# Kernel tuning notes

Hardware: AMD Instinct MI355X
Metric: run time of the kernel (lower is better)

Reference implementation:

```python
import math
import jax, jax.numpy as jnp
import numpy as np

N_HEADS = 16
D_EMBED = 1024
D_HEAD = D_EMBED // N_HEADS


def setup_inputs() -> dict:
    key = jax.random.key(0)
    k1, k2, k3, k4, k5 = jax.random.split(key, 5)
    B, S, D = 4, 2048, D_EMBED
    scale = 1.0 / math.sqrt(D)
    return {
        "x": jax.random.normal(k1, (B, S, D), dtype=jnp.float32),
        "in_proj_w": jax.random.normal(k2, (3 * D, D), dtype=jnp.float32) * scale,
        "in_proj_b": jax.random.normal(k3, (3 * D,), dtype=jnp.float32) * 0.02,
        "out_proj_w": jax.random.normal(k4, (D, D), dtype=jnp.float32) * scale,
        "out_proj_b": jax.random.normal(k5, (D,), dtype=jnp.float32) * 0.02,
        "causal_mask": 0,
    }


def reference(x, in_proj_w, in_proj_b, out_proj_w, out_proj_b, causal_mask):
    B, S, D = x.shape
    # in_proj: torch Linear -> x @ W^T + b, then chunk into q,k,v
    qkv = x @ in_proj_w.T + in_proj_b              # [B,S,3D]
    q, k, v = jnp.split(qkv, 3, axis=-1)
    # [B,S,D] -> [B,H,S,d]
    def heads(t):
        return t.reshape(B, S, N_HEADS, D_HEAD).transpose(0, 2, 1, 3)
    q, k, v = heads(q), heads(k), heads(v)
    weight = jnp.einsum("bhsd,bhtd->bhst", q, k)   # [B,H,S,S] materialized scores
    if causal_mask:
        mask = jnp.triu(jnp.ones((S, S), dtype=bool), k=1)
        weight = jnp.where(mask, -jnp.inf, weight)
    weight = jax.nn.softmax(weight / math.sqrt(D_HEAD), axis=-1)
    out = jnp.einsum("bhst,bhtd->bhsd", weight, v)  # [B,H,S,d]
    out = out.transpose(0, 2, 1, 3).reshape(B, S, D)
    return out @ out_proj_w.T + out_proj_b
```

## Files before the change

### kernel.cpp

```cpp
#include <hip/hip_runtime.h>

typedef unsigned short u16;
typedef _Float16 h8 __attribute__((ext_vector_type(8)));
typedef __fp16 fp16x2 __attribute__((ext_vector_type(2)));
typedef float f32x4 __attribute__((ext_vector_type(4)));

constexpr int B_ = 4, S_ = 2048, D_ = 1024, H_ = 16;

__device__ __forceinline__ void async16(const void* g, void* l) {
  __builtin_amdgcn_global_load_lds(
      (const __attribute__((address_space(1))) void*)g,
      (__attribute__((address_space(3))) void*)l, 16, 0, 0);
}

__device__ __forceinline__ unsigned pk2(float a, float b) {
  union { fp16x2 h; unsigned u; } c;
  c.h = __builtin_amdgcn_cvt_pkrtz(a, b);
  return c.u;
}

__device__ __forceinline__ float fexp2(float x) {
#if __has_builtin(__builtin_amdgcn_exp2f)
  return __builtin_amdgcn_exp2f(x);
#else
  return exp2f(x);
#endif
}

#define QSCALE 0.18033688011112042f

__global__ __launch_bounds__(256) void cvt3_kernel(
    const float* __restrict__ x, const float* __restrict__ wi,
    const float* __restrict__ wo, _Float16* __restrict__ xh,
    _Float16* __restrict__ wih, _Float16* __restrict__ woh)
{
  const int bid = blockIdx.x;
  const float* src;
  _Float16* dst;
  int base;
  if (bid < 8192)       { src = x;  dst = xh;  base = bid; }
  else if (bid < 11264) { src = wi; dst = wih; base = bid - 8192; }
  else                  { src = wo; dst = woh; base = bid - 11264; }
  const int i = (base * 256 + threadIdx.x) * 4;
  const float4 v = *(const float4*)(src + i);
  uint2 o;
  o.x = pk2(v.x, v.y);
  o.y = pk2(v.z, v.w);
  *(uint2*)(dst + i) = o;
}

template<bool OUT_HALF, bool SCALE_Q>
__global__ __launch_bounds__(256, 2) void gemm128p_f16(
    const _Float16* __restrict__ A, const _Float16* __restrict__ Bw,
    const float* __restrict__ bias, void* __restrict__ Cout,
    int M, int N, int K)
{
  __shared__ __align__(16) _Float16 sA[2][8192];
  __shared__ __align__(16) _Float16 sB[2][8192];

  const int tid = threadIdx.x;
  const int lane = tid & 63, w = tid >> 6;
  const int wm = w & 1, wn = w >> 1;

  const int id = blockIdx.x;
  const int cpx = gridDim.x >> 3;
  const int swz = (id & 7) * cpx + (id >> 3);
  const int nbx = N >> 7;
  const int bx = swz % nbx, by = swz / nbx;
  const int m0 = by * 128, n0 = bx * 128;

  const int r15 = lane & 15, s4 = lane >> 4;
  const int tA0 = w, tA1 = w + 4;
  const _Float16* gA0 = A + (size_t)(m0 + 16 * tA0 + r15) * K + s4 * 8;
  const _Float16* gA1 = A + (size_t)(m0 + 16 * tA1 + r15) * K + s4 * 8;
  const _Float16* gB0 = Bw + (size_t)(n0 + 16 * tA0 + r15) * K + s4 * 8;
  const _Float16* gB1 = Bw + (size_t)(n0 + 16 * tA1 + r15) * K + s4 * 8;

  auto stage = [&](int tile, int kk, int bq) {
    const int ko = tile * 64 + kk * 32;
    async16(gA0 + ko, &sA[bq][(tA0 * 2 + kk) * 512]);
    async16(gA1 + ko, &sA[bq][(tA1 * 2 + kk) * 512]);
    async16(gB0 + ko, &sB[bq][(tA0 * 2 + kk) * 512]);
    async16(gB1 + ko, &sB[bq][(tA1 * 2 + kk) * 512]);
  };

  const f32x4 zf = {0.f, 0.f, 0.f, 0.f};
  f32x4 acc[4][4];
#pragma unroll
  for (int i = 0; i < 4; ++i)
#pragma unroll
    for (int j = 0; j < 4; ++j) acc[i][j] = zf;

  const int NT = K >> 6;

  stage(0, 0, 0);
  stage(0, 1, 0);
  stage(1, 0, 1);

#define VM8 asm volatile("s_waitcnt vmcnt(8)" ::: "memory")
#define VM4 asm volatile("s_waitcnt vmcnt(4)" ::: "memory")
#define VM0 asm volatile("s_waitcnt vmcnt(0)" ::: "memory")
#define FENCE asm volatile("" ::: "memory")

  for (int T = 0; T < NT; ++T) {
    const int buf = T & 1;
    const bool lastT = (T == NT - 1);

    if (!lastT) { VM8; } else { VM4; }
    __builtin_amdgcn_s_barrier();
    FENCE;
    {
      h8 fa[4], fb[4];
#pragma unroll
      for (int i = 0; i < 4; ++i) {
        fa[i] = *(const h8*)&sA[buf][((wm * 4 + i) * 2 + 0) * 512 + lane * 8];
        fb[i] = *(const h8*)&sB[buf][((wn * 4 + i) * 2 + 0) * 512 + lane * 8];
      }
      if (T + 1 < NT) stage(T + 1, 1, (T + 1) & 1);
      __builtin_amdgcn_s_setprio(1);
#pragma unroll
      for (int i = 0; i < 4; ++i)
#pragma unroll
        for (int j = 0; j < 4; ++j)
          acc[i][j] = __builtin_amdgcn_mfma_f32_16x16x32_f16(fa[i], fb[j], acc[i][j], 0, 0, 0);
      __builtin_amdgcn_s_setprio(0);
    }

    if (!lastT) { VM8; } else { VM0; }
    __builtin_amdgcn_s_barrier();
    FENCE;
    {
      h8 fa[4], fb[4];
#pragma unroll
      for (int i = 0; i < 4; ++i) {
        fa[i] = *(const h8*)&sA[buf][((wm * 4 + i) * 2 + 1) * 512 + lane * 8];
        fb[i] = *(const h8*)&sB[buf][((wn * 4 + i) * 2 + 1) * 512 + lane * 8];
      }
      if (T + 2 < NT) stage(T + 2, 0, buf);
      __builtin_amdgcn_s_setprio(1);
#pragma unroll
      for (int i = 0; i < 4; ++i)
#pragma unroll
        for (int j = 0; j < 4; ++j)
          acc[i][j] = __builtin_amdgcn_mfma_f32_16x16x32_f16(fa[i], fb[j], acc[i][j], 0, 0, 0);
      __builtin_amdgcn_s_setprio(0);
    }
  }

#undef VM8
#undef VM4
#undef VM0
#undef FENCE

  const int g = lane >> 4, cc = lane & 15;
#pragma unroll
  for (int j = 0; j < 4; ++j) {
    const int col = n0 + (wn * 4 + j) * 16 + cc;
    const float bv = bias[col];
    float qs = 1.0f;
    if constexpr (SCALE_Q) qs = (col < 1024) ? QSCALE : 1.0f;
#pragma unroll
    for (int i = 0; i < 4; ++i) {
      const int rowb = m0 + (wm * 4 + i) * 16 + g * 4;
#pragma unroll
      for (int r = 0; r < 4; ++r) {
        float v = acc[i][j][r] + bv;
        if constexpr (SCALE_Q) v *= qs;
        if constexpr (OUT_HALF)
          ((_Float16*)Cout)[(size_t)(rowb + r) * N + col] = (_Float16)v;
        else
          ((float*)Cout)[(size_t)(rowb + r) * N + col] = v;
      }
    }
  }
}

__global__ __launch_bounds__(256) void transpose_v(
    const u16* __restrict__ qkv, u16* __restrict__ vT)
{
  __shared__ u16 T[64 * 73];
  const int tid = threadIdx.x;
  const int bh = blockIdx.y, s0 = blockIdx.x * 64;
  const int b = bh >> 4, h = bh & 15;
#pragma unroll
  for (int t = 0; t < 2; ++t) {
    const int c = tid + t * 256, r = c >> 3, cs = c & 7;
    union { int4 v; u16 s[8]; } u;
    u.v = *(const int4*)(qkv + (size_t)(b * S_ + s0 + r) * 3072 + 2048 + h * 64 + 8 * cs);
#pragma unroll
    for (int i = 0; i < 8; ++i) T[r * 73 + 8 * cs + i] = u.s[i];
  }
  __syncthreads();
#pragma unroll
  for (int t = 0; t < 2; ++t) {
    const int c = tid + t * 256, rd = c >> 3, ss = c & 7;
    union { int4 v; u16 s[8]; } u;
#pragma unroll
    for (int i = 0; i < 8; ++i) u.s[i] = T[(8 * ss + i) * 73 + rd];
    *(int4*)(vT + (size_t)(bh * 64 + rd) * S_ + s0 + 8 * ss) = u.v;
  }
}

__global__ __launch_bounds__(256, 4) void attn_f16(
    const _Float16* __restrict__ qkv, const _Float16* __restrict__ vT,
    _Float16* __restrict__ attnO, const int* __restrict__ causal_ptr)
{
  __shared__ __align__(16) _Float16 sQP[9216];
  __shared__ __align__(16) _Float16 sK[4096];
  __shared__ __align__(16) _Float16 sV[4096];

  const int tid = threadIdx.x, lane = tid & 63, w = tid >> 6;
  const int q4 = lane >> 4, cc = lane & 15;
  const int bh = blockIdx.y, b = bh >> 4, h = bh & 15;
  const int q0 = blockIdx.x * 128;
  const int causal = causal_ptr[0];

  {
    const int rr = lane & 15, sc8 = lane >> 4;
#pragma unroll
    for (int tt = 0; tt < 2; ++tt) {
      const int t = 2 * w + tt;
#pragma unroll
      for (int sh = 0; sh < 2; ++sh) {
        const _Float16* g = qkv + (size_t)(b * S_ + q0 + 16 * t + rr) * 3072 + h * 64 + 8 * (4 * sh + sc8);
        async16(g, &sQP[t * 1024 + sh * 512]);
      }
    }
  }
  __syncthreads();

  h8 qf[2][2];
#pragma unroll
  for (int m = 0; m < 2; ++m)
#pragma unroll
    for (int kk = 0; kk < 2; ++kk)
      qf[m][kk] = *(const h8*)&sQP[((2 * w + m) << 10) + (kk << 9) + (lane << 3)];

  h8 ones;
#pragma unroll
  for (int i = 0; i < 8; ++i) ones[i] = (_Float16)1.0f;

  const _Float16* gK = qkv + (size_t)(b * S_ + 16 * w + (lane & 15)) * 3072 + 1024 + h * 64 + 8 * (lane >> 4);
  const _Float16* gV = vT + (size_t)(bh * 64 + 16 * w + (lane & 15)) * S_ + 8 * (lane >> 4);
  _Float16* lK0 = &sK[w * 1024];
  _Float16* lV0 = &sV[w * 1024];

  const int wp = w * 2304;

  const f32x4 zf = {0.f, 0.f, 0.f, 0.f};
  f32x4 oa[2][4], lac[2];
#pragma unroll
  for (int m = 0; m < 2; ++m) {
    lac[m] = zf;
#pragma unroll
    for (int nt = 0; nt < 4; ++nt) oa[m][nt] = zf;
  }

  for (int j0 = 0; j0 < S_; j0 += 64) {
    if (causal && j0 > q0 + 127) break;
    __syncthreads();
    async16(gK + (size_t)j0 * 3072, lK0);
    async16(gK + (size_t)j0 * 3072 + 32, lK0 + 512);
    async16(gV + j0, lV0);
    async16(gV + j0 + 32, lV0 + 512);
    __syncthreads();

    f32x4 sc[2][4];
    __builtin_amdgcn_s_setprio(1);
#pragma unroll
    for (int nt = 0; nt < 4; ++nt) {
      const h8 kf0 = *(const h8*)&sK[(nt << 10) + (lane << 3)];
      const h8 kf1 = *(const h8*)&sK[(nt << 10) + 512 + (lane << 3)];
#pragma unroll
      for (int m = 0; m < 2; ++m) {
        sc[m][nt] = __builtin_amdgcn_mfma_f32_16x16x32_f16(kf0, qf[m][0], zf, 0, 0, 0);
        sc[m][nt] = __builtin_amdgcn_mfma_f32_16x16x32_f16(kf1, qf[m][1], sc[m][nt], 0, 0, 0);
      }
    }
    __builtin_amdgcn_s_setprio(0);

    if (causal) {
#pragma unroll
      for (int m = 0; m < 2; ++m)
#pragma unroll
        for (int nt = 0; nt < 4; ++nt)
#pragma unroll
          for (int r = 0; r < 4; ++r)
            if ((j0 + nt * 16 + q4 * 4 + r) > (q0 + 32 * w + m * 16 + cc))
              sc[m][nt][r] = -1.0e30f;
    }

#pragma unroll
    for (int m = 0; m < 2; ++m)
#pragma unroll
      for (int nt = 0; nt < 4; ++nt) {
        uint2 pk;
        pk.x = pk2(fexp2(sc[m][nt][0]), fexp2(sc[m][nt][1]));
        pk.y = pk2(fexp2(sc[m][nt][2]), fexp2(sc[m][nt][3]));
        *(uint2*)&sQP[wp + (m * 16 + cc) * 72 + nt * 16 + q4 * 4] = pk;
      }

    asm volatile("s_waitcnt lgkmcnt(0)" ::: "memory");

    h8 pf[2][2];
#pragma unroll
    for (int m = 0; m < 2; ++m)
#pragma unroll
      for (int kk = 0; kk < 2; ++kk)
        pf[m][kk] = *(const h8*)&sQP[wp + (m * 16 + cc) * 72 + kk * 32 + q4 * 8];

    __builtin_amdgcn_s_setprio(1);
#pragma unroll
    for (int m = 0; m < 2; ++m) {
      lac[m] = __builtin_amdgcn_mfma_f32_16x16x32_f16(pf[m][0], ones, lac[m], 0, 0, 0);
      lac[m] = __builtin_amdgcn_mfma_f32_16x16x32_f16(pf[m][1], ones, lac[m], 0, 0, 0);
    }
#pragma unroll
    for (int nt = 0; nt < 4; ++nt) {
      const h8 vf0 = *(const h8*)&sV[(nt << 10) + (lane << 3)];
      const h8 vf1 = *(const h8*)&sV[(nt << 10) + 512 + (lane << 3)];
#pragma unroll
      for (int m = 0; m < 2; ++m) {
        oa[m][nt] = __builtin_amdgcn_mfma_f32_16x16x32_f16(pf[m][0], vf0, oa[m][nt], 0, 0, 0);
        oa[m][nt] = __builtin_amdgcn_mfma_f32_16x16x32_f16(pf[m][1], vf1, oa[m][nt], 0, 0, 0);
      }
    }
    __builtin_amdgcn_s_setprio(0);
  }

#pragma unroll
  for (int m = 0; m < 2; ++m) {
    float inv[4];
#pragma unroll
    for (int r = 0; r < 4; ++r) inv[r] = 1.0f / lac[m][r];
#pragma unroll
    for (int nt = 0; nt < 4; ++nt) {
      const int col = h * 64 + nt * 16 + cc;
#pragma unroll
      for (int r = 0; r < 4; ++r) {
        const int row = b * S_ + q0 + 32 * w + m * 16 + q4 * 4 + r;
        attnO[(size_t)row * D_ + col] = (_Float16)(oa[m][nt][r] * inv[r]);
      }
    }
  }
}

extern "C" void kernel_launch(void* const* d_in, const int* in_sizes, int n_in,
                              void* d_out, int out_size, void* d_ws, size_t ws_size,
                              hipStream_t stream)
{
  const float* x  = (const float*)d_in[0];
  const float* wi = (const float*)d_in[1];
  const float* bi = (const float*)d_in[2];
  const float* wo = (const float*)d_in[3];
  const float* bo = (const float*)d_in[4];
  const int* causal = (const int*)d_in[5];

  _Float16* xh   = (_Float16*)d_ws;
  _Float16* wih  = xh + 8388608;
  _Float16* woh  = wih + 3145728;
  _Float16* qkvb = woh + 1048576;
  _Float16* vT   = qkvb + 25165824;
  _Float16* attn = vT + 8388608;

  const int M = B_ * S_;

  cvt3_kernel<<<12288, 256, 0, stream>>>(x, wi, wo, xh, wih, woh);

  gemm128p_f16<true, true><<<1536, 256, 0, stream>>>(
      xh, wih, bi, qkvb, M, 3 * D_, D_);

  transpose_v<<<dim3(32, 64), 256, 0, stream>>>((const u16*)qkvb, (u16*)vT);

  attn_f16<<<dim3(16, 64), 256, 0, stream>>>(qkvb, vT, attn, causal);

  gemm128p_f16<false, false><<<512, 256, 0, stream>>>(
      attn, woh, bo, d_out, M, D_, D_);
}
```

Baseline: 318.3 us.

## Fuse V transpose into QKV GEMM epilogue, simplify GEMM pipeline, swizzle attention LDS

The V part of the QKV projection is now written transposed straight from the GEMM epilogue, which removes the separate transpose_v kernel and its extra pass over V. The GEMM drops its hand-tuned double-buffered async pipeline for a single-buffer loop with two syncthreads per 64-wide K step. It also loses the occupancy hint in launch bounds. The attention kernel gets a 1D grid with block-index swizzling and an XOR-swizzled P tile in LDS instead of padding. The simpler GEMM loop may expose global load latency that the old pipeline hid.

New measurement: 313.0 us. About the same (-1.7%).

```diff
diff --git a/kernel.cpp b/kernel.cpp
--- a/kernel.cpp
+++ b/kernel.cpp
@@ -28,6 +28,8 @@
 }
 
 #define QSCALE 0.18033688011112042f
+
+#define LGKM0 asm volatile("s_waitcnt lgkmcnt(0)" ::: "memory")
 
 __global__ __launch_bounds__(256) void cvt3_kernel(
     const float* __restrict__ x, const float* __restrict__ wi,
@@ -49,14 +51,14 @@
   *(uint2*)(dst + i) = o;
 }
 
-template<bool OUT_HALF, bool SCALE_Q>
-__global__ __launch_bounds__(256, 2) void gemm128p_f16(
+template<bool OUT_HALF, bool SCALE_Q, bool FUSE_V>
+__global__ __launch_bounds__(256) void gemm128k64_f16(
     const _Float16* __restrict__ A, const _Float16* __restrict__ Bw,
     const float* __restrict__ bias, void* __restrict__ Cout,
-    int M, int N, int K)
+    _Float16* __restrict__ vTout, int M, int N, int K)
 {
-  __shared__ __align__(16) _Float16 sA[2][8192];
-  __shared__ __align__(16) _Float16 sB[2][8192];
+  __shared__ __align__(16) _Float16 sA[8192];
+  __shared__ __align__(16) _Float16 sB[8192];
 
   const int tid = threadIdx.x;
   const int lane = tid & 63, w = tid >> 6;
@@ -70,19 +72,16 @@
   const int m0 = by * 128, n0 = bx * 128;
 
   const int r15 = lane & 15, s4 = lane >> 4;
-  const int tA0 = w, tA1 = w + 4;
-  const _Float16* gA0 = A + (size_t)(m0 + 16 * tA0 + r15) * K + s4 * 8;
-  const _Float16* gA1 = A + (size_t)(m0 + 16 * tA1 + r15) * K + s4 * 8;
-  const _Float16* gB0 = Bw + (size_t)(n0 + 16 * tA0 + r15) * K + s4 * 8;
-  const _Float16* gB1 = Bw + (size_t)(n0 + 16 * tA1 + r15) * K + s4 * 8;
-
-  auto stage = [&](int tile, int kk, int bq) {
-    const int ko = tile * 64 + kk * 32;
-    async16(gA0 + ko, &sA[bq][(tA0 * 2 + kk) * 512]);
-    async16(gA1 + ko, &sA[bq][(tA1 * 2 + kk) * 512]);
-    async16(gB0 + ko, &sB[bq][(tA0 * 2 + kk) * 512]);
-    async16(gB1 + ko, &sB[bq][(tA1 * 2 + kk) * 512]);
-  };
+  const _Float16* gA[4];
+  const _Float16* gB[4];
+  int lo[4];
+#pragma unroll
+  for (int j = 0; j < 4; ++j) {
+    const int t = 2 * w + (j >> 1), kk = j & 1;
+    gA[j] = A + (size_t)(m0 + 16 * t + r15) * K + kk * 32 + s4 * 8;
+    gB[j] = Bw + (size_t)(n0 + 16 * t + r15) * K + kk * 32 + s4 * 8;
+    lo[j] = (t * 2 + kk) * 512;
+  }
 
   const f32x4 zf = {0.f, 0.f, 0.f, 0.f};
   f32x4 acc[4][4];
@@ -91,66 +90,34 @@
 #pragma unroll
     for (int j = 0; j < 4; ++j) acc[i][j] = zf;
 
-  const int NT = K >> 6;
-
-  stage(0, 0, 0);
-  stage(0, 1, 0);
-  stage(1, 0, 1);
-
-#define VM8 asm volatile("s_waitcnt vmcnt(8)" ::: "memory")
-#define VM4 asm volatile("s_waitcnt vmcnt(4)" ::: "memory")
-#define VM0 asm volatile("s_waitcnt vmcnt(0)" ::: "memory")
-#define FENCE asm volatile("" ::: "memory")
-
-  for (int T = 0; T < NT; ++T) {
-    const int buf = T & 1;
-    const bool lastT = (T == NT - 1);
-
-    if (!lastT) { VM8; } else { VM4; }
-    __builtin_amdgcn_s_barrier();
-    FENCE;
-    {
-      h8 fa[4], fb[4];
-#pragma unroll
-      for (int i = 0; i < 4; ++i) {
-        fa[i] = *(const h8*)&sA[buf][((wm * 4 + i) * 2 + 0) * 512 + lane * 8];
-        fb[i] = *(const h8*)&sB[buf][((wn * 4 + i) * 2 + 0) * 512 + lane * 8];
-      }
-      if (T + 1 < NT) stage(T + 1, 1, (T + 1) & 1);
-      __builtin_amdgcn_s_setprio(1);
-#pragma unroll
-      for (int i = 0; i < 4; ++i)
-#pragma unroll
-        for (int j = 0; j < 4; ++j)
-          acc[i][j] = __builtin_amdgcn_mfma_f32_16x16x32_f16(fa[i], fb[j], acc[i][j], 0, 0, 0);
-      __builtin_amdgcn_s_setprio(0);
-    }
-
-    if (!lastT) { VM8; } else { VM0; }
-    __builtin_amdgcn_s_barrier();
-    FENCE;
-    {
-      h8 fa[4], fb[4];
-#pragma unroll
-      for (int i = 0; i < 4; ++i) {
-        fa[i] = *(const h8*)&sA[buf][((wm * 4 + i) * 2 + 1) * 512 + lane * 8];
-        fb[i] = *(const h8*)&sB[buf][((wn * 4 + i) * 2 + 1) * 512 + lane * 8];
-      }
-      if (T + 2 < NT) stage(T + 2, 0, buf);
-      __builtin_amdgcn_s_setprio(1);
-#pragma unroll
-      for (int i = 0; i < 4; ++i)
-#pragma unroll
-        for (int j = 0; j < 4; ++j)
-          acc[i][j] = __builtin_amdgcn_mfma_f32_16x16x32_f16(fa[i], fb[j], acc[i][j], 0, 0, 0);
-      __builtin_amdgcn_s_setprio(0);
-    }
-  }
-
-#undef VM8
-#undef VM4
-#undef VM0
-#undef FENCE
+  for (int k0 = 0; k0 < K; k0 += 64) {
+    __syncthreads();
+#pragma unroll
+    for (int j = 0; j < 4; ++j) async16(gA[j] + k0, &sA[lo[j]]);
+#pragma unroll
+    for (int j = 0; j < 4; ++j) async16(gB[j] + k0, &sB[lo[j]]);
+    __syncthreads();
+
+    h8 fb[4][2];
+#pragma unroll
+    for (int j = 0; j < 4; ++j)
+#pragma unroll
+      for (int kk = 0; kk < 2; ++kk)
+        fb[j][kk] = *(const h8*)&sB[((wn * 4 + j) * 2 + kk) * 512 + lane * 8];
+
+    __builtin_amdgcn_s_setprio(1);
+#pragma unroll
+    for (int i = 0; i < 4; ++i) {
+      const h8 fa0 = *(const h8*)&sA[((wm * 4 + i) * 2 + 0) * 512 + lane * 8];
+      const h8 fa1 = *(const h8*)&sA[((wm * 4 + i) * 2 + 1) * 512 + lane * 8];
+#pragma unroll
+      for (int j = 0; j < 4; ++j) {
+        acc[i][j] = __builtin_amdgcn_mfma_f32_16x16x32_f16(fa0, fb[j][0], acc[i][j], 0, 0, 0);
+        acc[i][j] = __builtin_amdgcn_mfma_f32_16x16x32_f16(fa1, fb[j][1], acc[i][j], 0, 0, 0);
+      }
+    }
+    __builtin_amdgcn_s_setprio(0);
+  }
 
   const int g = lane >> 4, cc = lane & 15;
 #pragma unroll
@@ -162,42 +129,29 @@
 #pragma unroll
     for (int i = 0; i < 4; ++i) {
       const int rowb = m0 + (wm * 4 + i) * 16 + g * 4;
+      float vv[4];
 #pragma unroll
       for (int r = 0; r < 4; ++r) {
-        float v = acc[i][j][r] + bv;
-        if constexpr (SCALE_Q) v *= qs;
-        if constexpr (OUT_HALF)
-          ((_Float16*)Cout)[(size_t)(rowb + r) * N + col] = (_Float16)v;
-        else
-          ((float*)Cout)[(size_t)(rowb + r) * N + col] = v;
-      }
-    }
-  }
-}
-
-__global__ __launch_bounds__(256) void transpose_v(
-    const u16* __restrict__ qkv, u16* __restrict__ vT)
-{
-  __shared__ u16 T[64 * 73];
-  const int tid = threadIdx.x;
-  const int bh = blockIdx.y, s0 = blockIdx.x * 64;
-  const int b = bh >> 4, h = bh & 15;
-#pragma unroll
-  for (int t = 0; t < 2; ++t) {
-    const int c = tid + t * 256, r = c >> 3, cs = c & 7;
-    union { int4 v; u16 s[8]; } u;
-    u.v = *(const int4*)(qkv + (size_t)(b * S_ + s0 + r) * 3072 + 2048 + h * 64 + 8 * cs);
-#pragma unroll
-    for (int i = 0; i < 8; ++i) T[r * 73 + 8 * cs + i] = u.s[i];
-  }
-  __syncthreads();
-#pragma unroll
-  for (int t = 0; t < 2; ++t) {
-    const int c = tid + t * 256, rd = c >> 3, ss = c & 7;
-    union { int4 v; u16 s[8]; } u;
-#pragma unroll
-    for (int i = 0; i < 8; ++i) u.s[i] = T[(8 * ss + i) * 73 + rd];
-    *(int4*)(vT + (size_t)(bh * 64 + rd) * S_ + s0 + 8 * ss) = u.v;
+        vv[r] = acc[i][j][r] + bv;
+        if constexpr (SCALE_Q) vv[r] *= qs;
+      }
+      bool vcol = false;
+      if constexpr (FUSE_V) vcol = (col >= 2048);
+      if (vcol) {
+        union { _Float16 hx[4]; uint2 u; } pv;
+#pragma unroll
+        for (int r = 0; r < 4; ++r) pv.hx[r] = (_Float16)vv[r];
+        *(uint2*)&vTout[((size_t)(((rowb >> 11) << 10) + (col - 2048)) << 11) + (rowb & 2047)] = pv.u;
+      } else {
+#pragma unroll
+        for (int r = 0; r < 4; ++r) {
+          if constexpr (OUT_HALF)
+            ((_Float16*)Cout)[(size_t)(rowb + r) * N + col] = (_Float16)vv[r];
+          else
+            ((float*)Cout)[(size_t)(rowb + r) * N + col] = vv[r];
+        }
+      }
+    }
   }
 }
 
@@ -205,14 +159,16 @@
     const _Float16* __restrict__ qkv, const _Float16* __restrict__ vT,
     _Float16* __restrict__ attnO, const int* __restrict__ causal_ptr)
 {
-  __shared__ __align__(16) _Float16 sQP[9216];
+  __shared__ __align__(16) _Float16 sQP[8192];
   __shared__ __align__(16) _Float16 sK[4096];
   __shared__ __align__(16) _Float16 sV[4096];
 
   const int tid = threadIdx.x, lane = tid & 63, w = tid >> 6;
   const int q4 = lane >> 4, cc = lane & 15;
-  const int bh = blockIdx.y, b = bh >> 4, h = bh & 15;
-  const int q0 = blockIdx.x * 128;
+  const int id = blockIdx.x;
+  const int swz = (id & 7) * 128 + (id >> 3);
+  const int bh = swz >> 4, b = bh >> 4, h = bh & 15;
+  const int q0 = (swz & 15) << 7;
   const int causal = causal_ptr[0];
 
   {
@@ -245,7 +201,8 @@
   _Float16* lK0 = &sK[w * 1024];
   _Float16* lV0 = &sV[w * 1024];
 
-  const int wp = w * 2304;
+  const int wp = w * 2048;
+  const int psw = (cc & 7) << 3;
 
   const f32x4 zf = {0.f, 0.f, 0.f, 0.f};
   f32x4 oa[2][4], lac[2];
@@ -297,17 +254,17 @@
         uint2 pk;
         pk.x = pk2(fexp2(sc[m][nt][0]), fexp2(sc[m][nt][1]));
         pk.y = pk2(fexp2(sc[m][nt][2]), fexp2(sc[m][nt][3]));
-        *(uint2*)&sQP[wp + (m * 16 + cc) * 72 + nt * 16 + q4 * 4] = pk;
-      }
-
-    asm volatile("s_waitcnt lgkmcnt(0)" ::: "memory");
+        *(uint2*)&sQP[wp + ((m * 16 + cc) << 6) + ((nt * 16 + q4 * 4) ^ psw)] = pk;
+      }
+
+    LGKM0;
 
     h8 pf[2][2];
 #pragma unroll
     for (int m = 0; m < 2; ++m)
 #pragma unroll
       for (int kk = 0; kk < 2; ++kk)
-        pf[m][kk] = *(const h8*)&sQP[wp + (m * 16 + cc) * 72 + kk * 32 + q4 * 8];
+        pf[m][kk] = *(const h8*)&sQP[wp + ((m * 16 + cc) << 6) + ((kk * 32 + q4 * 8) ^ psw)];
 
     __builtin_amdgcn_s_setprio(1);
 #pragma unroll
@@ -367,13 +324,11 @@
 
   cvt3_kernel<<<12288, 256, 0, stream>>>(x, wi, wo, xh, wih, woh);
 
-  gemm128p_f16<true, true><<<1536, 256, 0, stream>>>(
-      xh, wih, bi, qkvb, M, 3 * D_, D_);
-
-  transpose_v<<<dim3(32, 64), 256, 0, stream>>>((const u16*)qkvb, (u16*)vT);
-
-  attn_f16<<<dim3(16, 64), 256, 0, stream>>>(qkvb, vT, attn, causal);
-
-  gemm128p_f16<false, false><<<512, 256, 0, stream>>>(
-      attn, woh, bo, d_out, M, D_, D_);
-}
+  gemm128k64_f16<true, true, true><<<1536, 256, 0, stream>>>(
+      xh, wih, bi, qkvb, vT, M, 3 * D_, D_);
+
+  attn_f16<<<1024, 256, 0, stream>>>(qkvb, vT, attn, causal);
+
+  gemm128k64_f16<false, false, false><<<512, 256, 0, stream>>>(
+      attn, woh, bo, d_out, nullptr, M, D_, D_);
+}
```
